# Performance work log

Measured on AMD Instinct MI355X. Metric: run time of the kernel, lower is better.

## Reference

```python
import jax, jax.numpy as jnp
import numpy as np

N, E, D, H, L = 4096, 131072, 2048, 4, 2  # nodes, edges, embed_dim, heads, layers
HD = D // H


def setup_inputs() -> dict:
    key = jax.random.key(0)
    ks = jax.random.split(key, 11)
    s = 0.02
    feats = jax.random.normal(ks[0], (N, D), jnp.float32)
    edge_index = jax.random.randint(ks[1], (E, 2), 0, N, dtype=jnp.int32)
    # per-layer linear params, stored as [in, out] so y = x @ W + b (== torch x @ W.T + b)
    Wq = jax.random.normal(ks[2], (L, D, D), jnp.float32) * s
    Wk = jax.random.normal(ks[3], (L, D, D), jnp.float32) * s
    Wv = jax.random.normal(ks[4], (L, D, D), jnp.float32) * s
    Wo = jax.random.normal(ks[5], (L, D, D), jnp.float32) * s
    bq = jnp.zeros((L, D), jnp.float32)
    bk = jnp.zeros((L, D), jnp.float32)
    bv = jnp.zeros((L, D), jnp.float32)
    bo = jnp.zeros((L, D), jnp.float32)
    return dict(feats=feats, Wq=Wq, bq=bq, Wk=Wk, bk=bk, Wv=Wv, bv=bv,
                Wo=Wo, bo=bo, edge_index=edge_index)


def _gnn_forward(feats, Wq, bq, Wk, bk, Wv, bv, Wo, bo, row, col):
    n = feats.shape[0]
    # dense edge mask [1, N, N] (masked_fill where mask == 0 -> -10000)
    mask = jnp.zeros((n, n), bool).at[row, col].set(True)[None]
    scale = 1.0 / jnp.sqrt(jnp.asarray(HD, feats.dtype))
    x = feats
    for l in range(L):
        q = (x @ Wq[l] + bq[l]).reshape(n, H, HD).transpose(1, 0, 2)  # [H,N,d]
        k = (x @ Wk[l] + bk[l]).reshape(n, H, HD).transpose(1, 0, 2)
        v = (x @ Wv[l] + bv[l]).reshape(n, H, HD).transpose(1, 0, 2)
        scores = jnp.einsum('hnd,hmd->hnm', q, k) * scale          # [H,N,N]
        scores = jnp.where(mask, scores, jnp.asarray(-10000.0, scores.dtype))
        attn = jax.nn.softmax(scores, axis=-1)                      # [H,N,N]
        se = attn[:, row, col]                                      # [H,E] gather per-edge
        out_e = se[:, :, None] * v[:, col]                          # [H,E,d]
        agg = jax.vmap(lambda o: jax.ops.segment_sum(o, row, num_segments=n))(out_e)  # [H,N,d]
        x = agg.transpose(1, 0, 2).reshape(n, H * HD) @ Wo[l] + bo[l]
    return x


def reference(feats, Wq, bq, Wk, bk, Wv, bv, Wo, bo, edge_index):
    row, col = edge_index[:, 0], edge_index[:, 1]
    return _gnn_forward(feats, Wq, bq, Wk, bk, Wv, bv, Wo, bo, row, col)
```

## Files before the change

### kernel.cpp

```cpp
#include <hip/hip_runtime.h>
#include <hip/hip_bf16.h>

typedef unsigned short u16;
typedef unsigned int u32;
typedef short bf16x8 __attribute__((ext_vector_type(8)));
typedef float f32x4 __attribute__((ext_vector_type(4)));
typedef unsigned short u16x4 __attribute__((ext_vector_type(4)));
typedef unsigned short u16x8 __attribute__((ext_vector_type(8)));
typedef float f32x4v __attribute__((ext_vector_type(4)));

#define NN 4096
#define DD 2048
#define HH 4
#define HDIM 512
#define EE 131072
#define NB 512
#define EBS 256
#define QS 6144
#define MAXDEG 256

__device__ __forceinline__ float bf2f(u16 x) {
    return __uint_as_float(((u32)x) << 16);
}
__device__ __forceinline__ u16 f2bf(float f) {
    u32 u = __float_as_uint(f);
    u += 0x7fffu + ((u >> 16) & 1u);
    return (u16)(u >> 16);
}

#define GLOAD16(g, l)                                                          \
    __builtin_amdgcn_global_load_lds(                                          \
        (const __attribute__((address_space(1))) void*)(g),                    \
        (__attribute__((address_space(3))) void*)(l), 16, 0, 0)

__global__ __launch_bounds__(256) void k_cvt(const float* __restrict__ in,
                                             u16* __restrict__ out, int n4)
{
    int i = blockIdx.x * 256 + threadIdx.x;
    if (i >= n4) return;
    f32x4v v = *(const f32x4v*)&in[i * 4];
    u16x4 o;
#pragma unroll
    for (int j = 0; j < 4; j++) o[j] = f2bf(v[j]);
    *(u16x4*)&out[i * 4] = o;
}

template <bool OUTF32>
__global__ __launch_bounds__(256, 2) void k_gemm(
    const u16* __restrict__ A, const u16* __restrict__ Bt,
    const float* __restrict__ bias0, const float* __restrict__ bias1,
    const float* __restrict__ bias2, void* __restrict__ Cout,
    int M, int Ncols, int K)
{
    extern __shared__ u16 lds[];
    u16* sA = lds;
    u16* sB = lds + 3 * 8192;

    int t = threadIdx.x;
    int wid = t >> 6, lane = t & 63;
    int wr = wid >> 1, wc = wid & 1;
    int l15 = lane & 15, kg = lane >> 4;

    int flat = blockIdx.y * gridDim.x + blockIdx.x;
    int per = (gridDim.x * gridDim.y) >> 3;
    int nid = (flat & 7) * per + (flat >> 3);
    int gy = gridDim.y;
    int bm = nid % gy;
    int bn = nid / gy;

    const int NT = K >> 5;

    int trow = t >> 2;
    int scolE = ((t & 3) ^ ((t >> 3) & 3)) * 8;
    const u16* Abase = A + ((size_t)bm * 256 + trow) * K + scolE;
    const u16* Bbase = Bt + ((size_t)bn * 128 + trow) * K + scolE;

#define STAGE_A(buf, TT, j)                                                    \
    GLOAD16(Abase + (size_t)(j) * 64 * K + (size_t)(TT) * 32,                  \
            sA + (buf) * 8192 + (j) * 2048 + t * 8)
#define STAGE_B(buf, TT, j)                                                    \
    GLOAD16(Bbase + (size_t)(j) * 64 * K + (size_t)(TT) * 32,                  \
            sB + (buf) * 4096 + (j) * 2048 + t * 8)

    int sl = (kg ^ ((l15 >> 1) & 3)) * 8;

    f32x4 acc[8][4];
#pragma unroll
    for (int m = 0; m < 8; m++)
#pragma unroll
        for (int n = 0; n < 4; n++) acc[m][n] = (f32x4){0.f, 0.f, 0.f, 0.f};

#pragma unroll
    for (int j = 0; j < 4; j++) STAGE_A(0, 0, j);
    STAGE_B(0, 0, 0); STAGE_B(0, 0, 1);
#pragma unroll
    for (int j = 0; j < 4; j++) STAGE_A(1, 1, j);
    STAGE_B(1, 1, 0); STAGE_B(1, 1, 1);
    asm volatile("s_waitcnt vmcnt(6)" ::: "memory");
    __builtin_amdgcn_s_barrier();

    int bufc = 0;
    for (int T = 0; T < NT; ++T) {
        const u16* bA = sA + bufc * 8192;
        const u16* bB = sB + bufc * 4096;
        int nxt2 = bufc + 2; if (nxt2 >= 3) nxt2 -= 3;
        if (T + 2 < NT) {
#pragma unroll
            for (int j = 0; j < 4; j++) STAGE_A(nxt2, T + 2, j);
            STAGE_B(nxt2, T + 2, 0); STAGE_B(nxt2, T + 2, 1);
        }
        bf16x8 bfr[4], afr[8];
#pragma unroll
        for (int n = 0; n < 4; ++n)
            bfr[n] = *(const bf16x8*)(bB + (wc * 64 + n * 16 + l15) * 32 + sl);
#pragma unroll
        for (int m = 0; m < 8; ++m)
            afr[m] = *(const bf16x8*)(bA + (wr * 128 + m * 16 + l15) * 32 + sl);
        __builtin_amdgcn_s_setprio(1);
#pragma unroll
        for (int m = 0; m < 8; ++m)
#pragma unroll
            for (int n = 0; n < 4; ++n)
                acc[m][n] = __builtin_amdgcn_mfma_f32_16x16x32_bf16(
                    afr[m], bfr[n], acc[m][n], 0, 0, 0);
        __builtin_amdgcn_s_setprio(0);
        if (T + 2 < NT)
            asm volatile("s_waitcnt vmcnt(6)" ::: "memory");
        else if (T + 1 < NT)
            asm volatile("s_waitcnt vmcnt(0)" ::: "memory");
        __builtin_amdgcn_s_barrier();
        bufc += 1; if (bufc >= 3) bufc -= 3;
    }
#undef STAGE_A
#undef STAGE_B

    int row0 = bm * 256 + wr * 128 + kg * 4;
    int col0 = bn * 128 + wc * 64 + l15;
#pragma unroll
    for (int n = 0; n < 4; n++) {
        int cc = col0 + n * 16;
        int sel = cc >> 11;
        const float* bp = (sel == 0) ? bias0 : (sel == 1) ? bias1 : bias2;
        float bv = bp[cc & 2047];
#pragma unroll
        for (int m = 0; m < 8; m++) {
            int rb = row0 + m * 16;
#pragma unroll
            for (int r = 0; r < 4; r++) {
                float v = acc[m][n][r] + bv;
                if (OUTF32)
                    ((float*)Cout)[(size_t)(rb + r) * Ncols + cc] = v;
                else
                    ((u16*)Cout)[(size_t)(rb + r) * Ncols + cc] = f2bf(v);
            }
        }
    }
}

__global__ void k_wtrans(const float* __restrict__ Wq, const float* __restrict__ Wk,
                         const float* __restrict__ Wv, const float* __restrict__ Wo,
                         int loff, u16* __restrict__ Wt)
{
    int z = blockIdx.z;
    const float* W = (z == 0) ? Wq : (z == 1) ? Wk : (z == 2) ? Wv : Wo;
    u16* out = Wt + (size_t)z * DD * DD;
    __shared__ u16 tile[32][33];
    int tx = threadIdx.x, ty = threadIdx.y;
    int x = blockIdx.x * 32 + tx;
    int y0 = blockIdx.y * 32;
#pragma unroll
    for (int j = 0; j < 32; j += 8)
        tile[ty + j][tx] = f2bf(W[loff + (size_t)(y0 + ty + j) * DD + x]);
    __syncthreads();
    int ox = blockIdx.y * 32 + tx;
    int oy0 = blockIdx.x * 32;
#pragma unroll
    for (int j = 0; j < 32; j += 8)
        out[(size_t)(oy0 + ty + j) * DD + ox] = tile[tx][ty + j];
}

__global__ __launch_bounds__(256) void k_hist(const int* __restrict__ ei,
                                              int* __restrict__ blockcnt)
{
    __shared__ int h[NN];
    int b = blockIdx.x, t = threadIdx.x;
    for (int i = t; i < NN; i += 256) h[i] = 0;
    __syncthreads();
    int2 e = ((const int2*)ei)[b * EBS + t];
    atomicAdd(&h[e.x], 1);
    __syncthreads();
    for (int i = t; i < NN; i += 256) blockcnt[(size_t)b * NN + i] = h[i];
}

__global__ void k_rowscan(int* __restrict__ blockcnt, int* __restrict__ rowsum)
{
    int i = blockIdx.x * 256 + threadIdx.x;
    int run = 0;
    for (int b = 0; b < NB; b++) {
        int v = blockcnt[(size_t)b * NN + i];
        blockcnt[(size_t)b * NN + i] = run;
        run += v;
    }
    rowsum[i] = run;
}

__global__ __launch_bounds__(1024) void k_scan2(const int* __restrict__ rowsum,
                                                int* __restrict__ rstart)
{
    __shared__ int sh[1024];
    int t = threadIdx.x;
    int v[4], pre[4], s = 0;
#pragma unroll
    for (int j = 0; j < 4; j++) v[j] = rowsum[t * 4 + j];
#pragma unroll
    for (int j = 0; j < 4; j++) { pre[j] = s; s += v[j]; }
    sh[t] = s;
    __syncthreads();
    for (int off = 1; off < 1024; off <<= 1) {
        int x = (t >= off) ? sh[t - off] : 0;
        __syncthreads();
        sh[t] += x;
        __syncthreads();
    }
    int bp = (t == 0) ? 0 : sh[t - 1];
#pragma unroll
    for (int j = 0; j < 4; j++) rstart[t * 4 + j] = bp + pre[j];
    if (t == 1023) rstart[NN] = sh[1023];
}

__global__ __launch_bounds__(256) void k_scatter2(
    const int* __restrict__ ei, const int* __restrict__ blockcnt,
    const int* __restrict__ rstart, int* __restrict__ srow,
    int* __restrict__ scol)
{
    __shared__ int rsh[EBS];
    int b = blockIdx.x, t = threadIdx.x;
    int2 e = ((const int2*)ei)[b * EBS + t];
    rsh[t] = e.x;
    __syncthreads();
    int rank = 0;
    for (int j = 0; j < t; j++) rank += (rsh[j] == e.x);
    int pos = rstart[e.x] + blockcnt[(size_t)b * NN + e.x] + rank;
    srow[pos] = e.x;
    scol[pos] = e.y;
}

__global__ __launch_bounds__(64) void k_sortrow(int* __restrict__ scol,
                                                const int* __restrict__ rstart,
                                                int* __restrict__ flags)
{
    int i = blockIdx.x;
    int start = rstart[i], end = rstart[i + 1];
    int d = end - start;
    if (d <= 0) return;
    __shared__ int sc[1024];
    __shared__ int so[1024];
    int lane = threadIdx.x;
    for (int j = lane; j < d; j += 64) sc[j] = scol[start + j];
    __syncthreads();
    for (int j = lane; j < d; j += 64) {
        int cj = sc[j];
        int rank = 0;
        for (int q = 0; q < d; ++q) {
            int cq = sc[q];
            rank += (cq < cj) || (cq == cj && q < j);
        }
        so[rank] = cj;
    }
    __syncthreads();
    for (int j = lane; j < d; j += 64) {
        scol[start + j] = so[j];
        flags[start + j] = (j == 0) || (so[j] != so[j - 1]);
    }
}

__global__ __launch_bounds__(256) void k_edge(
    const u16* __restrict__ QKV, const int* __restrict__ scol,
    const int* __restrict__ flags, const int* __restrict__ rstart,
    u16* __restrict__ Aggb)
{
    int i = blockIdx.x;
    int start = rstart[i], end = rstart[i + 1];
    int deg = end - start;
    if (deg > MAXDEG) deg = MAXDEG;
    int t = threadIdx.x;
    int wid = t >> 6, lane = t & 63;
    int h = lane >> 4, l16 = lane & 15;

    __shared__ float pexpS[MAXDEG * HH];
    __shared__ float sinv[HH];
    __shared__ int scolS[MAXDEG];

    for (int j = t; j < deg; j += 256) scolS[j] = scol[start + j];

    const u16* qrow = QKV + (size_t)i * QS + h * HDIM + l16 * 8;
    u16x8 qreg[4];
#pragma unroll
    for (int ch = 0; ch < 4; ++ch) qreg[ch] = *(const u16x8*)(qrow + ch * 128);
    __syncthreads();

    const float scale = 0.04419417382415922f;

    for (int j = wid; j < deg; j += 4) {
        int c = scolS[j];
        const u16* krow = QKV + (size_t)c * QS + DD + h * HDIM + l16 * 8;
        float sx = 0.f, sy = 0.f;
#pragma unroll
        for (int ch = 0; ch < 4; ++ch) {
            u16x8 k8 = *(const u16x8*)(krow + ch * 128);
#pragma unroll
            for (int jj = 0; jj < 8; jj += 2) {
                sx += bf2f(qreg[ch][jj]) * bf2f(k8[jj]);
                sy += bf2f(qreg[ch][jj + 1]) * bf2f(k8[jj + 1]);
            }
        }
        float s = sx + sy;
#pragma unroll
        for (int off = 1; off < 16; off <<= 1) s += __shfl_xor(s, off, 64);
        if (l16 == 0) pexpS[j * HH + h] = expf(s * scale);
    }
    __syncthreads();

    {
        float dsum = 0.f;
        for (int j = lane; j < deg; j += 64)
            if (flags[start + j]) dsum += pexpS[j * HH + wid];
#pragma unroll
        for (int off = 32; off > 0; off >>= 1) dsum += __shfl_xor(dsum, off, 64);
        if (lane == 0) sinv[wid] = (deg > 0) ? 1.0f / dsum : 0.0f;
    }
    __syncthreads();

    float inv = sinv[wid];
    float acc[8] = {0.f, 0.f, 0.f, 0.f, 0.f, 0.f, 0.f, 0.f};
    const u16* Vcol = QKV + 2 * DD + wid * HDIM + lane * 8;
    int j = 0;
    for (; j + 2 <= deg; j += 2) {
        int c0 = scolS[j], c1 = scolS[j + 1];
        u16x8 v0 = *(const u16x8*)(Vcol + (size_t)c0 * QS);
        u16x8 v1 = *(const u16x8*)(Vcol + (size_t)c1 * QS);
        float w0 = pexpS[j * HH + wid] * inv;
        float w1 = pexpS[(j + 1) * HH + wid] * inv;
#pragma unroll
        for (int e = 0; e < 8; e++) acc[e] += w0 * bf2f(v0[e]);
#pragma unroll
        for (int e = 0; e < 8; e++) acc[e] += w1 * bf2f(v1[e]);
    }
    if (j < deg) {
        int c0 = scolS[j];
        u16x8 v0 = *(const u16x8*)(Vcol + (size_t)c0 * QS);
        float w0 = pexpS[j * HH + wid] * inv;
#pragma unroll
        for (int e = 0; e < 8; e++) acc[e] += w0 * bf2f(v0[e]);
    }
    u16x8 o;
#pragma unroll
    for (int e = 0; e < 8; e++) o[e] = f2bf(acc[e]);
    *(u16x8*)&Aggb[(size_t)i * DD + wid * HDIM + lane * 8] = o;
}

extern "C" void kernel_launch(void* const* d_in, const int* in_sizes, int n_in,
                              void* d_out, int out_size, void* d_ws, size_t ws_size,
                              hipStream_t stream)
{
    const float* feats = (const float*)d_in[0];
    const float* Wq = (const float*)d_in[1];
    const float* bq = (const float*)d_in[2];
    const float* Wk = (const float*)d_in[3];
    const float* bk = (const float*)d_in[4];
    const float* Wv = (const float*)d_in[5];
    const float* bv = (const float*)d_in[6];
    const float* Wo = (const float*)d_in[7];
    const float* bo = (const float*)d_in[8];
    const int* ei = (const int*)d_in[9];
    float* out = (float*)d_out;

    size_t off = 0;
    auto alloc = [&](size_t bytes) {
        void* p = (char*)d_ws + off;
        off += (bytes + 255) & ~(size_t)255;
        return p;
    };
    const size_t ND = (size_t)NN * DD;
    u16* Xb = (u16*)alloc(ND * 2);
    u16* QKV = (u16*)alloc((size_t)NN * QS * 2);
    u16* Ab = (u16*)alloc(ND * 2);
    u16* Wt = (u16*)alloc((size_t)4 * DD * DD * 2);
    int* blockcnt = (int*)alloc((size_t)NB * NN * 4);
    int* rowsum = (int*)alloc((size_t)NN * 4);
    int* rstart = (int*)alloc((size_t)(NN + 1) * 4);
    int* srow = (int*)alloc((size_t)EE * 4);
    int* scol = (int*)alloc((size_t)EE * 4);
    int* flags = (int*)alloc((size_t)EE * 4);
    (void)ws_size; (void)in_sizes; (void)n_in; (void)out_size;

    const int GEMM_LDS = 3 * (8192 + 4096) * 2;
    hipFuncSetAttribute((const void*)k_gemm<false>,
                        hipFuncAttributeMaxDynamicSharedMemorySize, GEMM_LDS);
    hipFuncSetAttribute((const void*)k_gemm<true>,
                        hipFuncAttributeMaxDynamicSharedMemorySize, GEMM_LDS);

    k_hist<<<NB, 256, 0, stream>>>(ei, blockcnt);
    k_rowscan<<<NN / 256, 256, 0, stream>>>(blockcnt, rowsum);
    k_scan2<<<1, 1024, 0, stream>>>(rowsum, rstart);
    k_scatter2<<<NB, 256, 0, stream>>>(ei, blockcnt, rstart, srow, scol);
    k_sortrow<<<NN, 64, 0, stream>>>(scol, rstart, flags);

    k_cvt<<<(int)(ND / 4 / 256), 256, 0, stream>>>(feats, Xb, (int)(ND / 4));

    dim3 gqkv(QS / 128, NN / 256);
    dim3 go(DD / 128, NN / 256);
    for (int l = 0; l < 2; ++l) {
        k_wtrans<<<dim3(DD / 32, DD / 32, 4), dim3(32, 8), 0, stream>>>(
            Wq, Wk, Wv, Wo, l * DD * DD, Wt);
        k_gemm<false><<<gqkv, 256, GEMM_LDS, stream>>>(
            Xb, Wt, bq + l * DD, bk + l * DD, bv + l * DD, QKV, NN, QS, DD);
        k_edge<<<NN, 256, 0, stream>>>(QKV, scol, flags, rstart, Ab);
        if (l == 1) {
            k_gemm<true><<<go, 256, GEMM_LDS, stream>>>(
                Ab, Wt + 3 * (size_t)DD * DD, bo + l * DD, bo + l * DD, bo + l * DD, out, NN, DD, DD);
        } else {
            k_gemm<false><<<go, 256, GEMM_LDS, stream>>>(
                Ab, Wt + 3 * (size_t)DD * DD, bo + l * DD, bo + l * DD, bo + l * DD, Xb, NN, DD, DD);
        }
    }
}
```

Before: 646.7 us.

## Fuse score and V aggregation into one pass per edge in k_edge

The edge kernel now loads K and V for each neighbor in the same loop, computes the unnormalized exp score and immediately accumulates p*V into 32 per-lane registers. Partial sums from the four warps are reduced through a padded shared-memory buffer and normalized by the masked denominator afterwards. This drops the second sweep over neighbors and the dependent reload of column indices and weights. In exchange it adds register pressure (32 accumulators plus K/V buffers), roughly 33 KB of extra shared memory that may lower occupancy, and a cross-warp reduction step.

```diff
diff --git a/kernel.cpp b/kernel.cpp
--- a/kernel.cpp
+++ b/kernel.cpp
@@ -290,35 +290,55 @@
     __shared__ float pexpS[MAXDEG * HH];
     __shared__ float sinv[HH];
     __shared__ int scolS[MAXDEG];
+    __shared__ float part[4][64][33];
 
     for (int j = t; j < deg; j += 256) scolS[j] = scol[start + j];
 
-    const u16* qrow = QKV + (size_t)i * QS + h * HDIM + l16 * 8;
+    const u16* qrow = QKV + (size_t)i * QS + h * HDIM + l16 * 32;
     u16x8 qreg[4];
 #pragma unroll
-    for (int ch = 0; ch < 4; ++ch) qreg[ch] = *(const u16x8*)(qrow + ch * 128);
+    for (int ch = 0; ch < 4; ++ch) qreg[ch] = *(const u16x8*)(qrow + ch * 8);
     __syncthreads();
 
     const float scale = 0.04419417382415922f;
+    const u16* Kbase = QKV + DD + h * HDIM + l16 * 32;
+    const u16* Vbase = QKV + 2 * DD + h * HDIM + l16 * 32;
+
+    float acc[32];
+#pragma unroll
+    for (int d = 0; d < 32; ++d) acc[d] = 0.f;
 
     for (int j = wid; j < deg; j += 4) {
         int c = scolS[j];
-        const u16* krow = QKV + (size_t)c * QS + DD + h * HDIM + l16 * 8;
+        const u16* kr = Kbase + (size_t)c * QS;
+        const u16* vr = Vbase + (size_t)c * QS;
+        u16x8 k8[4], v8[4];
+#pragma unroll
+        for (int ch = 0; ch < 4; ++ch) k8[ch] = *(const u16x8*)(kr + ch * 8);
+#pragma unroll
+        for (int ch = 0; ch < 4; ++ch) v8[ch] = *(const u16x8*)(vr + ch * 8);
         float sx = 0.f, sy = 0.f;
 #pragma unroll
-        for (int ch = 0; ch < 4; ++ch) {
-            u16x8 k8 = *(const u16x8*)(krow + ch * 128);
+        for (int ch = 0; ch < 4; ++ch)
 #pragma unroll
             for (int jj = 0; jj < 8; jj += 2) {
-                sx += bf2f(qreg[ch][jj]) * bf2f(k8[jj]);
-                sy += bf2f(qreg[ch][jj + 1]) * bf2f(k8[jj + 1]);
+                sx += bf2f(qreg[ch][jj]) * bf2f(k8[ch][jj]);
+                sy += bf2f(qreg[ch][jj + 1]) * bf2f(k8[ch][jj + 1]);
             }
-        }
         float s = sx + sy;
 #pragma unroll
         for (int off = 1; off < 16; off <<= 1) s += __shfl_xor(s, off, 64);
-        if (l16 == 0) pexpS[j * HH + h] = expf(s * scale);
-    }
+        float p = expf(s * scale);
+        if (l16 == 0) pexpS[j * HH + h] = p;
+#pragma unroll
+        for (int ch = 0; ch < 4; ++ch)
+#pragma unroll
+            for (int e = 0; e < 8; ++e)
+                acc[ch * 8 + e] += p * bf2f(v8[ch][e]);
+    }
+
+#pragma unroll
+    for (int d = 0; d < 32; ++d) part[wid][lane][d] = acc[d];
     __syncthreads();
 
     {
@@ -331,32 +351,16 @@
     }
     __syncthreads();
 
-    float inv = sinv[wid];
-    float acc[8] = {0.f, 0.f, 0.f, 0.f, 0.f, 0.f, 0.f, 0.f};
-    const u16* Vcol = QKV + 2 * DD + wid * HDIM + lane * 8;
-    int j = 0;
-    for (; j + 2 <= deg; j += 2) {
-        int c0 = scolS[j], c1 = scolS[j + 1];
-        u16x8 v0 = *(const u16x8*)(Vcol + (size_t)c0 * QS);
-        u16x8 v1 = *(const u16x8*)(Vcol + (size_t)c1 * QS);
-        float w0 = pexpS[j * HH + wid] * inv;
-        float w1 = pexpS[(j + 1) * HH + wid] * inv;
-#pragma unroll
-        for (int e = 0; e < 8; e++) acc[e] += w0 * bf2f(v0[e]);
-#pragma unroll
-        for (int e = 0; e < 8; e++) acc[e] += w1 * bf2f(v1[e]);
-    }
-    if (j < deg) {
-        int c0 = scolS[j];
-        u16x8 v0 = *(const u16x8*)(Vcol + (size_t)c0 * QS);
-        float w0 = pexpS[j * HH + wid] * inv;
-#pragma unroll
-        for (int e = 0; e < 8; e++) acc[e] += w0 * bf2f(v0[e]);
-    }
+    float inv = sinv[h];
     u16x8 o;
 #pragma unroll
-    for (int e = 0; e < 8; e++) o[e] = f2bf(acc[e]);
-    *(u16x8*)&Aggb[(size_t)i * DD + wid * HDIM + lane * 8] = o;
+    for (int e = 0; e < 8; ++e) {
+        int d = wid * 8 + e;
+        float s = part[0][lane][d] + part[1][lane][d] +
+                  part[2][lane][d] + part[3][lane][d];
+        o[e] = f2bf(s * inv);
+    }
+    *(u16x8*)&Aggb[(size_t)i * DD + h * HDIM + l16 * 32 + wid * 8] = o;
 }
 
 extern "C" void kernel_launch(void* const* d_in, const int* in_sizes, int n_in,
@@ -395,10 +399,10 @@
     (void)ws_size; (void)in_sizes; (void)n_in; (void)out_size;
 
     const int GEMM_LDS = 3 * (8192 + 4096) * 2;
-    hipFuncSetAttribute((const void*)k_gemm<false>,
-                        hipFuncAttributeMaxDynamicSharedMemorySize, GEMM_LDS);
-    hipFuncSetAttribute((const void*)k_gemm<true>,
-                        hipFuncAttributeMaxDynamicSharedMemorySize, GEMM_LDS);
+    (void)hipFuncSetAttribute((const void*)k_gemm<false>,
+                              hipFuncAttributeMaxDynamicSharedMemorySize, GEMM_LDS);
+    (void)hipFuncSetAttribute((const void*)k_gemm<true>,
+                              hipFuncAttributeMaxDynamicSharedMemorySize, GEMM_LDS);
 
     k_hist<<<NB, 256, 0, stream>>>(ei, blockcnt);
     k_rowscan<<<NN / 256, 256, 0, stream>>>(blockcnt, rowsum);
```

After: 677.2 us. 1.05x slower.
